# Kernel tuning notes

Measured on AMD Instinct MI355X. Metric: run time of the kernel, lower is better.

Reference implementation:

```python
import jax, jax.numpy as jnp
import numpy as np

N_NODES = 50000
N_EDGES = 800000
IN_DIM = 64
H_DIM = 64


def setup_inputs() -> dict:
    key = jax.random.key(0)
    ks = jax.random.split(key, 6)
    feat = jax.random.normal(ks[0], (N_NODES, IN_DIM), dtype=jnp.float32)
    W1 = jax.random.normal(ks[1], (IN_DIM, H_DIM), dtype=jnp.float32) * (1.0 / np.sqrt(IN_DIM))
    b1 = jnp.zeros((H_DIM,), dtype=jnp.float32)
    W2 = jax.random.normal(ks[2], (H_DIM, 1), dtype=jnp.float32) * (1.0 / np.sqrt(H_DIM))
    b2 = jnp.zeros((1,), dtype=jnp.float32)
    src = jax.random.randint(ks[3], (N_EDGES,), 0, N_NODES, dtype=jnp.int32)
    dst = jax.random.randint(ks[4], (N_EDGES,), 0, N_NODES, dtype=jnp.int32)
    return {"feat": feat, "W1": W1, "b1": b1, "W2": W2, "b2": b2, "src": src, "dst": dst}


def _norms(src, dst, n_nodes):
    # DGL GraphConv norm='both': symmetric D^{-1/2} A D^{-1/2}, degrees clamped to >=1
    ones = jnp.ones(src.shape[0], dtype=jnp.float32)
    out_deg = jax.ops.segment_sum(ones, src, num_segments=n_nodes)
    in_deg = jax.ops.segment_sum(ones, dst, num_segments=n_nodes)
    out_norm = jax.lax.rsqrt(jnp.clip(out_deg, 1.0))
    in_norm = jax.lax.rsqrt(jnp.clip(in_deg, 1.0))
    return out_norm, in_norm


def _graph_conv(feat, W, b, src, dst, out_norm, in_norm, act):
    h = feat * out_norm[:, None]          # scale source features by D_out^{-1/2}
    msg = h[src]                          # gather along edges [E, d]
    agg = jax.ops.segment_sum(msg, dst, num_segments=feat.shape[0])  # scatter-sum to dst
    agg = agg * in_norm[:, None]          # scale by D_in^{-1/2}
    return act(agg @ W + b)


def reference(feat, W1, b1, W2, b2, src, dst):
    out_norm, in_norm = _norms(src, dst, feat.shape[0])
    h = _graph_conv(feat, W1, b1, src, dst, out_norm, in_norm, jax.nn.relu)
    return _graph_conv(h, W2, b2, src, dst, out_norm, in_norm, jax.nn.sigmoid)
```

## Files before the change

kernel.cpp:

```cpp
#include <hip/hip_runtime.h>
#include <hip/hip_fp16.h>
#include <math.h>


#define BS 256
#define EPB 4096

__global__ void hist_kernel(const int* __restrict__ src, const int* __restrict__ dst,
                            int* __restrict__ dstBinCount, int* __restrict__ srcBinCount,
                            int E, int NB) {
    __shared__ int histD[256];
    __shared__ int histS[256];
    int tid = threadIdx.x;
    histD[tid] = 0; histS[tid] = 0;
    __syncthreads();
    int base = blockIdx.x * EPB;
    #pragma unroll
    for (int it = 0; it < EPB / BS; it++) {
        int e = base + it * BS + tid;
        if (e < E) {
            atomicAdd(&histD[dst[e] >> 8], 1);
            atomicAdd(&histS[src[e] >> 8], 1);
        }
    }
    __syncthreads();
    if (tid < NB) {
        if (histD[tid]) atomicAdd(&dstBinCount[tid], histD[tid]);
        if (histS[tid]) atomicAdd(&srcBinCount[tid], histS[tid]);
    }
}

__global__ void scan_bins_kernel(const int* __restrict__ dstBinCount, const int* __restrict__ srcBinCount,
                                 int* __restrict__ dstBinBase, int* __restrict__ srcBinBase,
                                 int* __restrict__ dstCursor, int* __restrict__ srcCursor, int NB) {
    __shared__ int s[256];
    int t = threadIdx.x;
    int v = (t < NB) ? dstBinCount[t] : 0;
    s[t] = v; __syncthreads();
    for (int off = 1; off < 256; off <<= 1) {
        int u = (t >= off) ? s[t - off] : 0; __syncthreads();
        s[t] += u; __syncthreads();
    }
    if (t < NB) {
        int ex = s[t] - v;
        dstBinBase[t] = ex; dstCursor[t] = ex;
        if (t == NB - 1) dstBinBase[NB] = s[t];
    }
    __syncthreads();
    v = (t < NB) ? srcBinCount[t] : 0;
    s[t] = v; __syncthreads();
    for (int off = 1; off < 256; off <<= 1) {
        int u = (t >= off) ? s[t - off] : 0; __syncthreads();
        s[t] += u; __syncthreads();
    }
    if (t < NB) {
        int ex = s[t] - v;
        srcBinBase[t] = ex; srcCursor[t] = ex;
        if (t == NB - 1) srcBinBase[NB] = s[t];
    }
}

__global__ void partition_kernel(const int* __restrict__ src, const int* __restrict__ dst,
                                 int* __restrict__ dstCursor, int* __restrict__ srcCursor,
                                 int* __restrict__ packed, unsigned char* __restrict__ srcPart,
                                 int E, int NB) {
    __shared__ int curD[256];
    __shared__ int curS[256];
    int tid = threadIdx.x;
    int base = blockIdx.x * EPB;
    int dv[EPB / BS], sv[EPB / BS];
    curD[tid] = 0; curS[tid] = 0;
    __syncthreads();
    #pragma unroll
    for (int it = 0; it < EPB / BS; it++) {
        int e = base + it * BS + tid;
        if (e < E) {
            dv[it] = dst[e]; sv[it] = src[e];
            atomicAdd(&curD[dv[it] >> 8], 1);
            atomicAdd(&curS[sv[it] >> 8], 1);
        } else dv[it] = -1;
    }
    __syncthreads();
    int hD = curD[tid], hS = curS[tid];
    int rbD = (tid < NB && hD) ? atomicAdd(&dstCursor[tid], hD) : 0;
    int rbS = (tid < NB && hS) ? atomicAdd(&srcCursor[tid], hS) : 0;
    __syncthreads();
    curD[tid] = rbD; curS[tid] = rbS;
    __syncthreads();
    #pragma unroll
    for (int it = 0; it < EPB / BS; it++) {
        if (dv[it] >= 0) {
            int d = dv[it], s2 = sv[it];
            int pos = atomicAdd(&curD[d >> 8], 1);
            packed[pos] = s2 | ((d & 255) << 17);
            int pos2 = atomicAdd(&curS[s2 >> 8], 1);
            srcPart[pos2] = (unsigned char)(s2 & 255);
        }
    }
}

__global__ void finalize_kernel(const int* __restrict__ dstBinBase, const int* __restrict__ srcBinBase,
                                const int* __restrict__ packed, const unsigned char* __restrict__ srcPart,
                                int* __restrict__ csr_src, int* __restrict__ in_deg,
                                int* __restrict__ row_start, float* __restrict__ out_norm,
                                int N, int NB) {
    __shared__ int hist[256];
    __shared__ int sc[256];
    int tid = threadIdx.x;
    int b = blockIdx.x;
    if (b < NB) {
        int lo = dstBinBase[b], hi = dstBinBase[b + 1];
        hist[tid] = 0; __syncthreads();
        for (int i = lo + tid; i < hi; i += BS)
            atomicAdd(&hist[(packed[i] >> 17) & 255], 1);
        __syncthreads();
        int v = hist[tid];
        sc[tid] = v; __syncthreads();
        for (int off = 1; off < 256; off <<= 1) {
            int u = (tid >= off) ? sc[tid - off] : 0; __syncthreads();
            sc[tid] += u; __syncthreads();
        }
        int ex = sc[tid] - v;
        int n = b * 256 + tid;
        if (n < N) { in_deg[n] = v; row_start[n] = lo + ex; }
        sc[tid] = lo + ex;
        __syncthreads();
        for (int i = lo + tid; i < hi; i += BS) {
            int pv = packed[i];
            int pos = atomicAdd(&sc[(pv >> 17) & 255], 1);
            csr_src[pos] = pv & 0x1FFFF;
        }
    } else {
        int sb = b - NB;
        int lo = srcBinBase[sb], hi = srcBinBase[sb + 1];
        hist[tid] = 0; __syncthreads();
        for (int i = lo + tid; i < hi; i += BS)
            atomicAdd(&hist[srcPart[i]], 1);
        __syncthreads();
        int n = sb * 256 + tid;
        if (n < N) out_norm[n] = rsqrtf(fmaxf((float)hist[tid], 1.0f));
    }
}

__global__ void featw1_kernel(const float* __restrict__ feat,
                              const float* __restrict__ W1,
                              const float* __restrict__ out_norm,
                              __half* __restrict__ featp, int N) {
    __shared__ float w[64 * 64];
    int tid = threadIdx.x;
    for (int i = tid; i < 64 * 16; i += BS)
        ((float4*)w)[i] = ((const float4*)W1)[i];
    __syncthreads();
    int wave = tid >> 6, lane = tid & 63;
    int row = blockIdx.x * 4 + wave;
    if (row >= N) return;
    const float4* fr = (const float4*)(feat + (size_t)row * 64);
    float acc = 0.0f;
    #pragma unroll
    for (int k4 = 0; k4 < 16; k4++) {
        float4 a = fr[k4];
        acc += a.x * w[(4 * k4 + 0) * 64 + lane];
        acc += a.y * w[(4 * k4 + 1) * 64 + lane];
        acc += a.z * w[(4 * k4 + 2) * 64 + lane];
        acc += a.w * w[(4 * k4 + 3) * 64 + lane];
    }
    featp[(size_t)row * 64 + lane] = __float2half(out_norm[row] * acc);
}

__global__ void csr_agg1_kernel(const int* __restrict__ row_start, const int* __restrict__ in_deg,
                                const int* __restrict__ csr_src,
                                const __half* __restrict__ featp,
                                const float* __restrict__ b1, const float* __restrict__ W2,
                                const float* __restrict__ out_norm,
                                float* __restrict__ s_buf, int N) {
    int gid = blockIdx.x * blockDim.x + threadIdx.x;
    int n = gid >> 6;
    if (n >= N) return;
    int lane = threadIdx.x & 63;
    int g = lane >> 3;
    int l = lane & 7;
    int start = row_start[n];
    int deg = in_deg[n];
    float acc[8] = {0, 0, 0, 0, 0, 0, 0, 0};
    const uint4* fp4 = (const uint4*)featp;
    for (int j = 0; j < deg; j += 16) {
        int e0 = j + g;
        int e1 = j + 8 + g;
        bool p0 = e0 < deg;
        bool p1 = e1 < deg;
        int sn0 = p0 ? csr_src[start + e0] : 0;
        int sn1 = p1 ? csr_src[start + e1] : 0;
        uint4 q0 = {0, 0, 0, 0}, q1 = {0, 0, 0, 0};
        if (p0) q0 = fp4[(size_t)sn0 * 8 + l];
        if (p1) q1 = fp4[(size_t)sn1 * 8 + l];
        const __half2* h0 = (const __half2*)&q0;
        const __half2* h1 = (const __half2*)&q1;
        #pragma unroll
        for (int c = 0; c < 4; c++) {
            float2 f0 = __half22float2(h0[c]);
            float2 f1 = __half22float2(h1[c]);
            acc[2 * c]     += f0.x + f1.x;
            acc[2 * c + 1] += f0.y + f1.y;
        }
    }
    #pragma unroll
    for (int off = 8; off < 64; off <<= 1) {
        #pragma unroll
        for (int c = 0; c < 8; c++)
            acc[c] += __shfl_xor(acc[c], off, 64);
    }
    float inn = rsqrtf(fmaxf((float)deg, 1.0f));
    float v = 0.0f;
    #pragma unroll
    for (int c = 0; c < 8; c++) {
        float h = fmaxf(inn * acc[c] + b1[l * 8 + c], 0.0f);
        v += h * W2[l * 8 + c];
    }
    #pragma unroll
    for (int off = 1; off < 8; off <<= 1)
        v += __shfl_xor(v, off, 64);
    if (lane == 0)
        s_buf[n] = out_norm[n] * v;
}

__global__ void csr_agg2_kernel(const int* __restrict__ row_start, const int* __restrict__ in_deg,
                                const int* __restrict__ csr_src,
                                const float* __restrict__ s_buf, const float* __restrict__ b2,
                                float* __restrict__ out, int N) {
    int gid = blockIdx.x * blockDim.x + threadIdx.x;
    int n = gid >> 4;
    if (n >= N) return;
    int sub = gid & 15;
    int start = row_start[n];
    int deg = in_deg[n];
    float a = 0.0f;
    for (int j = sub; j < deg; j += 32) {
        int j1 = j + 16;
        int i0 = csr_src[start + j];
        int i1 = (j1 < deg) ? csr_src[start + j1] : 0;
        float v0 = s_buf[i0];
        float v1 = (j1 < deg) ? s_buf[i1] : 0.0f;
        a += v0 + v1;
    }
    #pragma unroll
    for (int off = 1; off < 16; off <<= 1)
        a += __shfl_xor(a, off, 64);
    if (sub == 0) {
        float x = rsqrtf(fmaxf((float)deg, 1.0f)) * a + b2[0];
        out[n] = 1.0f / (1.0f + expf(-x));
    }
}

extern "C" void kernel_launch(void* const* d_in, const int* in_sizes, int n_in,
                              void* d_out, int out_size, void* d_ws, size_t ws_size,
                              hipStream_t stream) {
    const float* feat = (const float*)d_in[0];
    const float* W1   = (const float*)d_in[1];
    const float* b1   = (const float*)d_in[2];
    const float* W2   = (const float*)d_in[3];
    const float* b2   = (const float*)d_in[4];
    const int* src = (const int*)d_in[5];
    const int* dst = (const int*)d_in[6];
    float* out = (float*)d_out;

    const int N  = in_sizes[0] / 64;
    const int E  = in_sizes[5];
    const int NB = (N + 255) >> 8;
    const int T  = (E + EPB - 1) / EPB;

    int* wsi = (int*)d_ws;
    int* dstBinCount = wsi;
    int* srcBinCount = dstBinCount + NB;
    int* dstBinBase  = srcBinCount + NB;
    int* srcBinBase  = dstBinBase + NB + 1;
    int* dstCursor   = srcBinBase + NB + 1;
    int* srcCursor   = dstCursor + NB;
    int* in_deg      = srcCursor + NB;
    int* row_start   = in_deg + N;
    int* packed      = row_start + N;
    int* csr_src     = packed + E;
    unsigned char* srcPart = (unsigned char*)(csr_src + E);
    size_t off_b = ((size_t)(6 * NB + 2) + 2 * (size_t)N + 2 * (size_t)E) * sizeof(int) + (size_t)E;
    off_b = (off_b + 15) & ~(size_t)15;
    __half* featp   = (__half*)((char*)d_ws + off_b);
    float*  out_norm = (float*)((char*)d_ws + off_b + (size_t)64 * N * sizeof(__half));
    float*  s_buf    = out_norm + N;

    hipMemsetAsync(dstBinCount, 0, (size_t)2 * NB * sizeof(int), stream);

    hist_kernel<<<T, BS, 0, stream>>>(src, dst, dstBinCount, srcBinCount, E, NB);
    scan_bins_kernel<<<1, 256, 0, stream>>>(
        dstBinCount, srcBinCount, dstBinBase, srcBinBase, dstCursor, srcCursor, NB);
    partition_kernel<<<T, BS, 0, stream>>>(
        src, dst, dstCursor, srcCursor, packed, srcPart, E, NB);
    finalize_kernel<<<2 * NB, BS, 0, stream>>>(
        dstBinBase, srcBinBase, packed, srcPart, csr_src, in_deg, row_start, out_norm, N, NB);
    featw1_kernel<<<(N + 3) / 4, BS, 0, stream>>>(feat, W1, out_norm, featp, N);
    csr_agg1_kernel<<<(int)(((size_t)N * 64 + BS - 1) / BS), BS, 0, stream>>>(
        row_start, in_deg, csr_src, featp, b1, W2, out_norm, s_buf, N);
    csr_agg2_kernel<<<(int)(((size_t)N * 16 + BS - 1) / BS), BS, 0, stream>>>(
        row_start, in_deg, csr_src, s_buf, b2, out, N);
}
```

Before: 189.6 us.

## Fuse all GCN stages into one persistent kernel with global barriers

```diff
diff --git a/kernel.cpp b/kernel.cpp
--- a/kernel.cpp
+++ b/kernel.cpp
@@ -3,118 +3,173 @@
 #include <math.h>
 
 
-#define BS 256
-#define EPB 4096
-
-__global__ void hist_kernel(const int* __restrict__ src, const int* __restrict__ dst,
-                            int* __restrict__ dstBinCount, int* __restrict__ srcBinCount,
-                            int E, int NB) {
-    __shared__ int histD[256];
-    __shared__ int histS[256];
-    int tid = threadIdx.x;
-    histD[tid] = 0; histS[tid] = 0;
+#define BS   256
+#define NBLK 512
+#define NBAR 8
+
+__device__ __forceinline__ void gbar(int* bar, int phase) {
     __syncthreads();
-    int base = blockIdx.x * EPB;
-    #pragma unroll
-    for (int it = 0; it < EPB / BS; it++) {
-        int e = base + it * BS + tid;
-        if (e < E) {
-            atomicAdd(&histD[dst[e] >> 8], 1);
-            atomicAdd(&histS[src[e] >> 8], 1);
-        }
+    if (threadIdx.x == 0) {
+        __threadfence();
+        __hip_atomic_fetch_add(&bar[(blockIdx.x & (NBAR - 1)) * 32], 1,
+                               __ATOMIC_RELAXED, __HIP_MEMORY_SCOPE_AGENT);
+        const int target = NBLK * phase;
+        int sum;
+        do {
+            sum = 0;
+            #pragma unroll
+            for (int i = 0; i < NBAR; i++)
+                sum += __hip_atomic_load(&bar[i * 32], __ATOMIC_RELAXED,
+                                         __HIP_MEMORY_SCOPE_AGENT);
+        } while (sum < target);
+        __threadfence();
+    }
+    __syncthreads();
+}
+
+__global__ __launch_bounds__(BS, 2) void gcn_persist(
+    const float* __restrict__ feat, const float* __restrict__ W1,
+    const float* __restrict__ b1, const float* __restrict__ W2,
+    const float* __restrict__ b2, const int* __restrict__ src,
+    const int* __restrict__ dst,
+    int* bar, int* countsD, int* countsS, int* rowSumD, int* rowSumS,
+    int* dstBinBase, int* srcBinBase, int* packed, unsigned char* srcPart,
+    int* csr_src, int* in_deg, int* row_start, float* out_norm, float* s_buf,
+    __half* featp, float* out, int N, int E, int NB)
+{
+    __shared__ float w[64 * 64];
+    __shared__ int hA[256];
+    __shared__ int hB[256];
+    __shared__ int sc[256];
+    __shared__ int rbD[256];
+    __shared__ int rbS[256];
+    __shared__ int curD[256];
+    __shared__ int curS[256];
+    __shared__ float onorm[256];
+
+    const int tid  = threadIdx.x;
+    const int b    = blockIdx.x;
+    const int wv   = tid >> 6;
+    const int lane = tid & 63;
+    const int EB   = (E + NBLK - 1) / NBLK;
+    const int elo  = b * EB;
+    const int ehi  = (elo + EB < E) ? elo + EB : E;
+
+    hA[tid] = 0; hB[tid] = 0;
+    for (int i = tid; i < 64 * 16; i += BS)
+        ((float4*)w)[i] = ((const float4*)W1)[i];
+    __syncthreads();
+    for (int e = elo + tid; e < ehi; e += BS) {
+        atomicAdd(&hA[dst[e] >> 8], 1);
+        atomicAdd(&hB[src[e] >> 8], 1);
     }
     __syncthreads();
     if (tid < NB) {
-        if (histD[tid]) atomicAdd(&dstBinCount[tid], histD[tid]);
-        if (histS[tid]) atomicAdd(&srcBinCount[tid], histS[tid]);
-    }
-}
-
-__global__ void scan_bins_kernel(const int* __restrict__ dstBinCount, const int* __restrict__ srcBinCount,
-                                 int* __restrict__ dstBinBase, int* __restrict__ srcBinBase,
-                                 int* __restrict__ dstCursor, int* __restrict__ srcCursor, int NB) {
-    __shared__ int s[256];
-    int t = threadIdx.x;
-    int v = (t < NB) ? dstBinCount[t] : 0;
-    s[t] = v; __syncthreads();
-    for (int off = 1; off < 256; off <<= 1) {
-        int u = (t >= off) ? s[t - off] : 0; __syncthreads();
-        s[t] += u; __syncthreads();
-    }
-    if (t < NB) {
-        int ex = s[t] - v;
-        dstBinBase[t] = ex; dstCursor[t] = ex;
-        if (t == NB - 1) dstBinBase[NB] = s[t];
-    }
-    __syncthreads();
-    v = (t < NB) ? srcBinCount[t] : 0;
-    s[t] = v; __syncthreads();
-    for (int off = 1; off < 256; off <<= 1) {
-        int u = (t >= off) ? s[t - off] : 0; __syncthreads();
-        s[t] += u; __syncthreads();
-    }
-    if (t < NB) {
-        int ex = s[t] - v;
-        srcBinBase[t] = ex; srcCursor[t] = ex;
-        if (t == NB - 1) srcBinBase[NB] = s[t];
-    }
-}
-
-__global__ void partition_kernel(const int* __restrict__ src, const int* __restrict__ dst,
-                                 int* __restrict__ dstCursor, int* __restrict__ srcCursor,
-                                 int* __restrict__ packed, unsigned char* __restrict__ srcPart,
-                                 int E, int NB) {
-    __shared__ int curD[256];
-    __shared__ int curS[256];
-    int tid = threadIdx.x;
-    int base = blockIdx.x * EPB;
-    int dv[EPB / BS], sv[EPB / BS];
-    curD[tid] = 0; curS[tid] = 0;
-    __syncthreads();
-    #pragma unroll
-    for (int it = 0; it < EPB / BS; it++) {
-        int e = base + it * BS + tid;
-        if (e < E) {
-            dv[it] = dst[e]; sv[it] = src[e];
-            atomicAdd(&curD[dv[it] >> 8], 1);
-            atomicAdd(&curS[sv[it] >> 8], 1);
-        } else dv[it] = -1;
-    }
-    __syncthreads();
-    int hD = curD[tid], hS = curS[tid];
-    int rbD = (tid < NB && hD) ? atomicAdd(&dstCursor[tid], hD) : 0;
-    int rbS = (tid < NB && hS) ? atomicAdd(&srcCursor[tid], hS) : 0;
-    __syncthreads();
-    curD[tid] = rbD; curS[tid] = rbS;
-    __syncthreads();
-    #pragma unroll
-    for (int it = 0; it < EPB / BS; it++) {
-        if (dv[it] >= 0) {
-            int d = dv[it], s2 = sv[it];
+        countsD[(size_t)tid * NBLK + b] = hA[tid];
+        countsS[(size_t)tid * NBLK + b] = hB[tid];
+    }
+    for (int row = b * 4 + wv; row < N; row += NBLK * 4) {
+        const float4* fr = (const float4*)(feat + (size_t)row * 64);
+        float acc = 0.0f;
+        #pragma unroll
+        for (int k4 = 0; k4 < 16; k4++) {
+            float4 a = fr[k4];
+            acc += a.x * w[(4 * k4 + 0) * 64 + lane];
+            acc += a.y * w[(4 * k4 + 1) * 64 + lane];
+            acc += a.z * w[(4 * k4 + 2) * 64 + lane];
+            acc += a.w * w[(4 * k4 + 3) * 64 + lane];
+        }
+        featp[(size_t)row * 64 + lane] = __float2half(acc);
+    }
+    gbar(bar, 1);
+
+    if (b < 2 * NB) {
+        int* row = (b < NB) ? (countsD + (size_t)b * NBLK)
+                            : (countsS + (size_t)(b - NB) * NBLK);
+        int a0 = row[2 * tid], a1 = row[2 * tid + 1];
+        int s01 = a0 + a1;
+        sc[tid] = s01; __syncthreads();
+        for (int off = 1; off < 256; off <<= 1) {
+            int u = (tid >= off) ? sc[tid - off] : 0; __syncthreads();
+            sc[tid] += u; __syncthreads();
+        }
+        int ex = sc[tid] - s01;
+        row[2 * tid] = ex; row[2 * tid + 1] = ex + a0;
+        if (tid == 255) {
+            if (b < NB) rowSumD[b] = sc[255];
+            else        rowSumS[b - NB] = sc[255];
+        }
+    }
+    gbar(bar, 2);
+
+    {
+        int vD = (tid < NB) ? rowSumD[tid] : 0;
+        sc[tid] = vD; __syncthreads();
+        for (int off = 1; off < 256; off <<= 1) {
+            int u = (tid >= off) ? sc[tid - off] : 0; __syncthreads();
+            sc[tid] += u; __syncthreads();
+        }
+        rbD[tid] = sc[tid] - vD;
+        __syncthreads();
+        int vS = (tid < NB) ? rowSumS[tid] : 0;
+        sc[tid] = vS; __syncthreads();
+        for (int off = 1; off < 256; off <<= 1) {
+            int u = (tid >= off) ? sc[tid - off] : 0; __syncthreads();
+            sc[tid] += u; __syncthreads();
+        }
+        rbS[tid] = sc[tid] - vS;
+        __syncthreads();
+        if (b == 0) {
+            if (tid < NB) { dstBinBase[tid] = rbD[tid]; srcBinBase[tid] = rbS[tid]; }
+            if (tid == NB) {
+                dstBinBase[NB] = rbD[NB - 1] + rowSumD[NB - 1];
+                srcBinBase[NB] = rbS[NB - 1] + rowSumS[NB - 1];
+            }
+        }
+        if (tid < NB) {
+            curD[tid] = rbD[tid] + countsD[(size_t)tid * NBLK + b];
+            curS[tid] = rbS[tid] + countsS[(size_t)tid * NBLK + b];
+        }
+        __syncthreads();
+        for (int e = elo + tid; e < ehi; e += BS) {
+            int d = dst[e], s2 = src[e];
             int pos = atomicAdd(&curD[d >> 8], 1);
             packed[pos] = s2 | ((d & 255) << 17);
             int pos2 = atomicAdd(&curS[s2 >> 8], 1);
             srcPart[pos2] = (unsigned char)(s2 & 255);
         }
     }
-}
-
-__global__ void finalize_kernel(const int* __restrict__ dstBinBase, const int* __restrict__ srcBinBase,
-                                const int* __restrict__ packed, const unsigned char* __restrict__ srcPart,
-                                int* __restrict__ csr_src, int* __restrict__ in_deg,
-                                int* __restrict__ row_start, float* __restrict__ out_norm,
-                                int N, int NB) {
-    __shared__ int hist[256];
-    __shared__ int sc[256];
-    int tid = threadIdx.x;
-    int b = blockIdx.x;
+    gbar(bar, 3);
+
+    if (b < NB) {
+        int lo = srcBinBase[b], hi = srcBinBase[b + 1];
+        hA[tid] = 0; __syncthreads();
+        for (int i = lo + tid; i < hi; i += BS)
+            atomicAdd(&hA[srcPart[i]], 1);
+        __syncthreads();
+        float on = rsqrtf(fmaxf((float)hA[tid], 1.0f));
+        onorm[tid] = on;
+        int n = b * 256 + tid;
+        if (n < N) out_norm[n] = on;
+        __syncthreads();
+        __half2* base2 = (__half2*)(featp + (size_t)b * 256 * 64);
+        int rows = N - b * 256; if (rows > 256) rows = 256;
+        int cap = rows * 32;
+        for (int idx = tid; idx < cap; idx += BS) {
+            float s2 = onorm[idx >> 5];
+            float2 f = __half22float2(base2[idx]);
+            base2[idx] = __floats2half2_rn(f.x * s2, f.y * s2);
+        }
+    }
+    gbar(bar, 4);
+
     if (b < NB) {
         int lo = dstBinBase[b], hi = dstBinBase[b + 1];
-        hist[tid] = 0; __syncthreads();
+        hA[tid] = 0; __syncthreads();
         for (int i = lo + tid; i < hi; i += BS)
-            atomicAdd(&hist[(packed[i] >> 17) & 255], 1);
-        __syncthreads();
-        int v = hist[tid];
+            atomicAdd(&hA[(packed[i] >> 17) & 255], 1);
+        __syncthreads();
+        int v = hA[tid];
         sc[tid] = v; __syncthreads();
         for (int off = 1; off < 256; off <<= 1) {
             int u = (tid >= off) ? sc[tid - off] : 0; __syncthreads();
@@ -123,131 +178,84 @@
         int ex = sc[tid] - v;
         int n = b * 256 + tid;
         if (n < N) { in_deg[n] = v; row_start[n] = lo + ex; }
-        sc[tid] = lo + ex;
+        curD[tid] = lo + ex;
         __syncthreads();
         for (int i = lo + tid; i < hi; i += BS) {
             int pv = packed[i];
-            int pos = atomicAdd(&sc[(pv >> 17) & 255], 1);
+            int pos = atomicAdd(&curD[(pv >> 17) & 255], 1);
             csr_src[pos] = pv & 0x1FFFF;
         }
-    } else {
-        int sb = b - NB;
-        int lo = srcBinBase[sb], hi = srcBinBase[sb + 1];
-        hist[tid] = 0; __syncthreads();
-        for (int i = lo + tid; i < hi; i += BS)
-            atomicAdd(&hist[srcPart[i]], 1);
-        __syncthreads();
-        int n = sb * 256 + tid;
-        if (n < N) out_norm[n] = rsqrtf(fmaxf((float)hist[tid], 1.0f));
-    }
-}
-
-__global__ void featw1_kernel(const float* __restrict__ feat,
-                              const float* __restrict__ W1,
-                              const float* __restrict__ out_norm,
-                              __half* __restrict__ featp, int N) {
-    __shared__ float w[64 * 64];
-    int tid = threadIdx.x;
-    for (int i = tid; i < 64 * 16; i += BS)
-        ((float4*)w)[i] = ((const float4*)W1)[i];
-    __syncthreads();
-    int wave = tid >> 6, lane = tid & 63;
-    int row = blockIdx.x * 4 + wave;
-    if (row >= N) return;
-    const float4* fr = (const float4*)(feat + (size_t)row * 64);
-    float acc = 0.0f;
-    #pragma unroll
-    for (int k4 = 0; k4 < 16; k4++) {
-        float4 a = fr[k4];
-        acc += a.x * w[(4 * k4 + 0) * 64 + lane];
-        acc += a.y * w[(4 * k4 + 1) * 64 + lane];
-        acc += a.z * w[(4 * k4 + 2) * 64 + lane];
-        acc += a.w * w[(4 * k4 + 3) * 64 + lane];
-    }
-    featp[(size_t)row * 64 + lane] = __float2half(out_norm[row] * acc);
-}
-
-__global__ void csr_agg1_kernel(const int* __restrict__ row_start, const int* __restrict__ in_deg,
-                                const int* __restrict__ csr_src,
-                                const __half* __restrict__ featp,
-                                const float* __restrict__ b1, const float* __restrict__ W2,
-                                const float* __restrict__ out_norm,
-                                float* __restrict__ s_buf, int N) {
-    int gid = blockIdx.x * blockDim.x + threadIdx.x;
-    int n = gid >> 6;
-    if (n >= N) return;
-    int lane = threadIdx.x & 63;
-    int g = lane >> 3;
-    int l = lane & 7;
-    int start = row_start[n];
-    int deg = in_deg[n];
-    float acc[8] = {0, 0, 0, 0, 0, 0, 0, 0};
-    const uint4* fp4 = (const uint4*)featp;
-    for (int j = 0; j < deg; j += 16) {
-        int e0 = j + g;
-        int e1 = j + 8 + g;
-        bool p0 = e0 < deg;
-        bool p1 = e1 < deg;
-        int sn0 = p0 ? csr_src[start + e0] : 0;
-        int sn1 = p1 ? csr_src[start + e1] : 0;
-        uint4 q0 = {0, 0, 0, 0}, q1 = {0, 0, 0, 0};
-        if (p0) q0 = fp4[(size_t)sn0 * 8 + l];
-        if (p1) q1 = fp4[(size_t)sn1 * 8 + l];
-        const __half2* h0 = (const __half2*)&q0;
-        const __half2* h1 = (const __half2*)&q1;
-        #pragma unroll
-        for (int c = 0; c < 4; c++) {
-            float2 f0 = __half22float2(h0[c]);
-            float2 f1 = __half22float2(h1[c]);
-            acc[2 * c]     += f0.x + f1.x;
-            acc[2 * c + 1] += f0.y + f1.y;
-        }
-    }
-    #pragma unroll
-    for (int off = 8; off < 64; off <<= 1) {
-        #pragma unroll
-        for (int c = 0; c < 8; c++)
-            acc[c] += __shfl_xor(acc[c], off, 64);
-    }
-    float inn = rsqrtf(fmaxf((float)deg, 1.0f));
-    float v = 0.0f;
-    #pragma unroll
-    for (int c = 0; c < 8; c++) {
-        float h = fmaxf(inn * acc[c] + b1[l * 8 + c], 0.0f);
-        v += h * W2[l * 8 + c];
-    }
-    #pragma unroll
-    for (int off = 1; off < 8; off <<= 1)
-        v += __shfl_xor(v, off, 64);
-    if (lane == 0)
-        s_buf[n] = out_norm[n] * v;
-}
-
-__global__ void csr_agg2_kernel(const int* __restrict__ row_start, const int* __restrict__ in_deg,
-                                const int* __restrict__ csr_src,
-                                const float* __restrict__ s_buf, const float* __restrict__ b2,
-                                float* __restrict__ out, int N) {
-    int gid = blockIdx.x * blockDim.x + threadIdx.x;
-    int n = gid >> 4;
-    if (n >= N) return;
-    int sub = gid & 15;
-    int start = row_start[n];
-    int deg = in_deg[n];
-    float a = 0.0f;
-    for (int j = sub; j < deg; j += 32) {
-        int j1 = j + 16;
-        int i0 = csr_src[start + j];
-        int i1 = (j1 < deg) ? csr_src[start + j1] : 0;
-        float v0 = s_buf[i0];
-        float v1 = (j1 < deg) ? s_buf[i1] : 0.0f;
-        a += v0 + v1;
-    }
-    #pragma unroll
-    for (int off = 1; off < 16; off <<= 1)
-        a += __shfl_xor(a, off, 64);
-    if (sub == 0) {
-        float x = rsqrtf(fmaxf((float)deg, 1.0f)) * a + b2[0];
-        out[n] = 1.0f / (1.0f + expf(-x));
+    }
+    gbar(bar, 5);
+
+    {
+        int g = lane >> 3, l = lane & 7;
+        const uint4* fp4 = (const uint4*)featp;
+        for (int n = b * 4 + wv; n < N; n += NBLK * 4) {
+            int start = row_start[n];
+            int deg = in_deg[n];
+            float acc[8] = {0, 0, 0, 0, 0, 0, 0, 0};
+            for (int j = 0; j < deg; j += 16) {
+                int e0 = j + g, e1 = j + 8 + g;
+                bool p0 = e0 < deg, p1 = e1 < deg;
+                int sn0 = p0 ? csr_src[start + e0] : 0;
+                int sn1 = p1 ? csr_src[start + e1] : 0;
+                uint4 q0 = {0, 0, 0, 0}, q1 = {0, 0, 0, 0};
+                if (p0) q0 = fp4[(size_t)sn0 * 8 + l];
+                if (p1) q1 = fp4[(size_t)sn1 * 8 + l];
+                const __half2* h0 = (const __half2*)&q0;
+                const __half2* h1 = (const __half2*)&q1;
+                #pragma unroll
+                for (int c = 0; c < 4; c++) {
+                    float2 f0 = __half22float2(h0[c]);
+                    float2 f1 = __half22float2(h1[c]);
+                    acc[2 * c]     += f0.x + f1.x;
+                    acc[2 * c + 1] += f0.y + f1.y;
+                }
+            }
+            #pragma unroll
+            for (int off = 8; off < 64; off <<= 1) {
+                #pragma unroll
+                for (int c = 0; c < 8; c++)
+                    acc[c] += __shfl_xor(acc[c], off, 64);
+            }
+            float inn = rsqrtf(fmaxf((float)deg, 1.0f));
+            float v2 = 0.0f;
+            #pragma unroll
+            for (int c = 0; c < 8; c++) {
+                float h = fmaxf(inn * acc[c] + b1[l * 8 + c], 0.0f);
+                v2 += h * W2[l * 8 + c];
+            }
+            #pragma unroll
+            for (int off = 1; off < 8; off <<= 1)
+                v2 += __shfl_xor(v2, off, 64);
+            if (lane == 0) s_buf[n] = out_norm[n] * v2;
+        }
+    }
+    gbar(bar, 6);
+
+    {
+        int sid = (b * BS + tid) >> 4;
+        int sub = lane & 15;
+        for (int n = sid; n < N; n += NBLK * (BS / 16)) {
+            int start = row_start[n], deg = in_deg[n];
+            float a = 0.0f;
+            for (int j = sub; j < deg; j += 32) {
+                int j1 = j + 16;
+                int i0 = csr_src[start + j];
+                int i1 = (j1 < deg) ? csr_src[start + j1] : 0;
+                float v0 = s_buf[i0];
+                float v1 = (j1 < deg) ? s_buf[i1] : 0.0f;
+                a += v0 + v1;
+            }
+            #pragma unroll
+            for (int off = 1; off < 16; off <<= 1)
+                a += __shfl_xor(a, off, 64);
+            if (sub == 0) {
+                float x = rsqrtf(fmaxf((float)deg, 1.0f)) * a + b2[0];
+                out[n] = 1.0f / (1.0f + expf(-x));
+            }
+        }
     }
 }
 
@@ -266,38 +274,33 @@
     const int N  = in_sizes[0] / 64;
     const int E  = in_sizes[5];
     const int NB = (N + 255) >> 8;
-    const int T  = (E + EPB - 1) / EPB;
 
     int* wsi = (int*)d_ws;
-    int* dstBinCount = wsi;
-    int* srcBinCount = dstBinCount + NB;
-    int* dstBinBase  = srcBinCount + NB;
-    int* srcBinBase  = dstBinBase + NB + 1;
-    int* dstCursor   = srcBinBase + NB + 1;
-    int* srcCursor   = dstCursor + NB;
-    int* in_deg      = srcCursor + NB;
-    int* row_start   = in_deg + N;
-    int* packed      = row_start + N;
-    int* csr_src     = packed + E;
-    unsigned char* srcPart = (unsigned char*)(csr_src + E);
-    size_t off_b = ((size_t)(6 * NB + 2) + 2 * (size_t)N + 2 * (size_t)E) * sizeof(int) + (size_t)E;
+    int* bar        = wsi;
+    int* countsD    = bar + NBAR * 32;
+    int* countsS    = countsD + (size_t)NB * NBLK;
+    int* rowSumD    = countsS + (size_t)NB * NBLK;
+    int* rowSumS    = rowSumD + NB;
+    int* dstBinBase = rowSumS + NB;
+    int* srcBinBase = dstBinBase + NB + 1;
+    int* packed     = srcBinBase + NB + 1;
+    int* csr_src    = packed + E;
+    int* in_deg     = csr_src + E;
+    int* row_start  = in_deg + N;
+    unsigned char* srcPart = (unsigned char*)(row_start + N);
+    size_t off_b = ((size_t)NBAR * 32 + 2 * (size_t)NB * NBLK + 2 * NB +
+                    2 * (NB + 1) + 2 * (size_t)E + 2 * (size_t)N) * sizeof(int)
+                   + (size_t)E;
     off_b = (off_b + 15) & ~(size_t)15;
-    __half* featp   = (__half*)((char*)d_ws + off_b);
+    __half* featp    = (__half*)((char*)d_ws + off_b);
     float*  out_norm = (float*)((char*)d_ws + off_b + (size_t)64 * N * sizeof(__half));
     float*  s_buf    = out_norm + N;
 
-    hipMemsetAsync(dstBinCount, 0, (size_t)2 * NB * sizeof(int), stream);
-
-    hist_kernel<<<T, BS, 0, stream>>>(src, dst, dstBinCount, srcBinCount, E, NB);
-    scan_bins_kernel<<<1, 256, 0, stream>>>(
-        dstBinCount, srcBinCount, dstBinBase, srcBinBase, dstCursor, srcCursor, NB);
-    partition_kernel<<<T, BS, 0, stream>>>(
-        src, dst, dstCursor, srcCursor, packed, srcPart, E, NB);
-    finalize_kernel<<<2 * NB, BS, 0, stream>>>(
-        dstBinBase, srcBinBase, packed, srcPart, csr_src, in_deg, row_start, out_norm, N, NB);
-    featw1_kernel<<<(N + 3) / 4, BS, 0, stream>>>(feat, W1, out_norm, featp, N);
-    csr_agg1_kernel<<<(int)(((size_t)N * 64 + BS - 1) / BS), BS, 0, stream>>>(
-        row_start, in_deg, csr_src, featp, b1, W2, out_norm, s_buf, N);
-    csr_agg2_kernel<<<(int)(((size_t)N * 16 + BS - 1) / BS), BS, 0, stream>>>(
-        row_start, in_deg, csr_src, s_buf, b2, out, N);
+    hipMemsetAsync(bar, 0, (size_t)NBAR * 32 * sizeof(int), stream);
+
+    gcn_persist<<<NBLK, BS, 0, stream>>>(
+        feat, W1, b1, W2, b2, src, dst,
+        bar, countsD, countsS, rowSumD, rowSumS, dstBinBase, srcBinBase,
+        packed, srcPart, csr_src, in_deg, row_start, out_norm, s_buf,
+        featp, out, N, E, NB);
 }
```

Measured after the change: 401.4 us. 112% more time.
